# Optimization experiments

Measured on AMD Instinct MI355X. Metric: run time of the kernel, lower is better.

The kernel has to match this reference:

```python
import jax, jax.numpy as jnp
import numpy as np

EMBED_DIM = 128
BATCH = 8
SEQ = 2048


def setup_inputs() -> dict:
    key = jax.random.key(0)
    k1, k2, k3 = jax.random.split(key, 3)
    inputs = jax.random.normal(k1, (BATCH, SEQ, EMBED_DIM), dtype=jnp.float32)
    rotation_params = jax.random.normal(k2, (EMBED_DIM * 3,), dtype=jnp.float32)
    entangle_params = jax.random.normal(k3, (EMBED_DIM,), dtype=jnp.float32)
    return {"inputs": inputs, "rotation_params": rotation_params, "entangle_params": entangle_params}


def reference(inputs, rotation_params, entangle_params):
    d = inputs.shape[-1]
    rot = rotation_params.reshape(d, 3)          # [d, 3]
    ent = entangle_params.reshape(d, 1)          # [d, 1]
    query = inputs @ rot                         # [B, S, 3]
    key = inputs @ ent                           # [B, S, 1]
    # scores: [B, S, S], softmax over last axis
    logits = jnp.einsum('bsk,btk->bst', query, key) / jnp.sqrt(jnp.float32(d))
    scores = jax.nn.softmax(logits, axis=-1)
    return jnp.einsum('bst,btd->bsd', scores, inputs)  # [B, S, d]
```

## Files before the change

### kernel.cpp

```cpp
#include <hip/hip_runtime.h>
#include <cstddef>
#include <cstdint>

#define SS 2048
#define DD 128
#define NB 8

typedef _Float16 half8 __attribute__((ext_vector_type(8)));
typedef __fp16 fp16x2 __attribute__((ext_vector_type(2)));
typedef __attribute__((ext_vector_type(16))) float f32x16;

#if __has_builtin(__builtin_amdgcn_exp2f)
#define EXP2F(x) __builtin_amdgcn_exp2f(x)
#else
#define EXP2F(x) exp2f(x)
#endif

#define WS_A2   0
#define WS_KV   (NB*SS*4)
#define WS_XF   (2*NB*SS*4)
#define BATCH_B (SS*DD*2)
#define WS_NEED (size_t)(WS_XF + (size_t)NB*BATCH_B)
#define WS_KMX  (WS_XF)
#define WS_KMN  (WS_XF + 128)


__global__ __launch_bounds__(256) void prep(
    const float* __restrict__ X, const float* __restrict__ rotp,
    const float* __restrict__ entp, uint8_t* __restrict__ ws, int do_x) {
  __shared__ __align__(16) uint8_t lbuf[128 * 80];
  const int blk = blockIdx.x;
  const int b = blk & 7;
  const int rc = blk >> 3;
  const int tid = threadIdx.x;
  const int d4 = (tid & 31) * 4;
  float* a2out = (float*)(ws + WS_A2);
  float* kout = (float*)(ws + WS_KV);

  const float4 f0 = *reinterpret_cast<const float4*>(rotp + d4 * 3);
  const float4 f1 = *reinterpret_cast<const float4*>(rotp + d4 * 3 + 4);
  const float4 f2 = *reinterpret_cast<const float4*>(rotp + d4 * 3 + 8);
  const float rs0 = f0.x + f0.y + f0.z;
  const float rs1 = f0.w + f1.x + f1.y;
  const float rs2 = f1.z + f1.w + f2.x;
  const float rs3 = f2.y + f2.z + f2.w;
  const float4 e4 = *reinterpret_cast<const float4*>(entp + d4);

#pragma unroll
  for (int rnd = 0; rnd < 4; ++rnd) {
    const int t31 = rnd * 8 + (tid >> 5);
    const int tg = rc * 32 + t31;
    const float4 xv =
        *reinterpret_cast<const float4*>(X + ((size_t)b * SS + tg) * DD + d4);
    float av = xv.x * rs0 + xv.y * rs1 + xv.z * rs2 + xv.w * rs3;
    float kv = xv.x * e4.x + xv.y * e4.y + xv.z * e4.z + xv.w * e4.w;
#pragma unroll
    for (int off = 16; off > 0; off >>= 1) {
      av += __shfl_xor(av, off, 64);
      kv += __shfl_xor(kv, off, 64);
    }
    if ((tid & 31) == 0) {
      a2out[b * SS + tg] = av * (0.08838834764831845f * 1.4426950408889634f);
      kout[b * SS + tg] = kv;
    }
    if (do_x) {
      const float vv[4] = {xv.x, xv.y, xv.z, xv.w};
#pragma unroll
      for (int i = 0; i < 4; ++i)
        *reinterpret_cast<_Float16*>(lbuf + (d4 + i) * 80 + t31 * 2) =
            (_Float16)vv[i];
    }
  }

  if (do_x) {
    __syncthreads();
    const int T = rc >> 2;
    const int wfb = (rc & 3) * 2;
    uint8_t* outb = ws + WS_XF + (size_t)b * BATCH_B + (T * 8 + wfb) * 4096;
    const int nt = tid >> 6;
    const int lane = tid & 63;
    const int hh = lane >> 5;
    const int d = nt * 32 + (lane & 31);
#pragma unroll
    for (int wfl = 0; wfl < 2; ++wfl) {
      const half8 v = *reinterpret_cast<const half8*>(
          lbuf + d * 80 + (wfl * 16 + hh * 8) * 2);
      *reinterpret_cast<half8*>(outb + wfl * 4096 + nt * 1024 + lane * 16) = v;
    }
  }
}

__global__ __launch_bounds__(1024, 4) void attn_mfma(
    const uint8_t* __restrict__ ws, float* __restrict__ out) {
  __shared__ float comb[64 * 128];
  __shared__ float dl[16 * 32];
  __shared__ float smx[16], smn[16];
  const int tid = threadIdx.x;
  const int w = tid >> 6;
  const int lane = tid & 63;
  const int lm = lane & 31;
  const int h = lane >> 5;
  const int mh = w >> 3;
  const int ks = w & 7;
  const int blk = blockIdx.x;
  const int b = blk & 7;
  const int s0 = (blk >> 3) * 64;

  const float* a2 = (const float*)(ws + WS_A2) + b * SS;
  const float* kb = (const float*)(ws + WS_KV) + b * SS;
  const uint8_t* xf = ws + WS_XF + (size_t)b * BATCH_B;

  const float2 k2 = *reinterpret_cast<const float2*>(kb + tid * 2);
  float mx = fmaxf(k2.x, k2.y);
  float mn = fminf(k2.x, k2.y);
#pragma unroll
  for (int off = 32; off > 0; off >>= 1) {
    mx = fmaxf(mx, __shfl_xor(mx, off, 64));
    mn = fminf(mn, __shfl_xor(mn, off, 64));
  }
  if (lane == 0) { smx[w] = mx; smn[w] = mn; }
  const float ga = a2[s0 + mh * 32 + lm];
  __syncthreads();
  mx = smx[0]; mn = smn[0];
#pragma unroll
  for (int q = 1; q < 16; ++q) { mx = fmaxf(mx, smx[q]); mn = fminf(mn, smn[q]); }
  const float gm = fmaxf(ga * mx, ga * mn);
  float gden = 0.0f;

  f32x16 acc[4];
#pragma unroll
  for (int nt = 0; nt < 4; ++nt)
#pragma unroll
    for (int r = 0; r < 16; ++r) acc[nt][r] = 0.0f;

  const uint8_t* wb = xf + ks * 4096 + lane * 16;
  const float* kp0 = kb + ks * 16 + h * 8;

  half8 bfA[4], bfB[4];
#pragma unroll
  for (int nt = 0; nt < 4; ++nt)
    bfA[nt] = *reinterpret_cast<const half8*>(wb + nt * 1024);

#define ABODY(TT, BFP, BFN)                                                   \
  {                                                                           \
    if ((TT) + 1 < 16) {                                                      \
      const uint8_t* nb_ = wb + ((TT) + 1) * 32768;                           \
      _Pragma("unroll") for (int nt = 0; nt < 4; ++nt)                        \
          BFN[nt] = *reinterpret_cast<const half8*>(nb_ + nt * 1024);         \
    }                                                                         \
    const float* kp = kp0 + (TT) * 128;                                       \
    const float4 ka = *reinterpret_cast<const float4*>(kp);                   \
    const float4 kc = *reinterpret_cast<const float4*>(kp + 4);               \
    const float kv8[8] = {ka.x, ka.y, ka.z, ka.w, kc.x, kc.y, kc.z, kc.w};    \
    float e0[8];                                                              \
    _Pragma("unroll") for (int j = 0; j < 8; ++j) {                           \
      e0[j] = EXP2F(fmaf(ga, kv8[j], -gm));                                   \
      gden += e0[j];                                                          \
    }                                                                         \
    union { half8 v; fp16x2 p[4]; } wa;                                       \
    _Pragma("unroll") for (int q = 0; q < 4; ++q)                             \
        wa.p[q] = __builtin_amdgcn_cvt_pkrtz(e0[2 * q], e0[2 * q + 1]);       \
    __builtin_amdgcn_s_setprio(1);                                            \
    _Pragma("unroll") for (int nt = 0; nt < 4; ++nt)                          \
        acc[nt] = __builtin_amdgcn_mfma_f32_32x32x16_f16(wa.v, BFP[nt],       \
                                                         acc[nt], 0, 0, 0);   \
    __builtin_amdgcn_s_setprio(0);                                            \
  }

  for (int T = 0; T < 16; T += 2) {
    ABODY(T, bfA, bfB);
    ABODY(T + 1, bfB, bfA);
  }
#undef ABODY

  gden += __shfl_xor(gden, 32, 64);
  if (lane < 32) dl[w * 32 + lane] = gden;
#pragma unroll
  for (int p = 0; p < 8; ++p) {
    if (ks == p) {
#pragma unroll
      for (int nt = 0; nt < 4; ++nt)
#pragma unroll
        for (int r = 0; r < 16; ++r) {
          const int rr = (r & 3) + 8 * (r >> 2) + 4 * h;
          const int idx = (mh * 32 + rr) * 128 + nt * 32 + lm;
          if (p == 0) comb[idx] = acc[nt][r];
          else        comb[idx] += acc[nt][r];
        }
    }
    __syncthreads();
  }

  const int r = tid >> 4;
  const int cg = (tid & 15) * 8;
  const int rmh = r >> 5, rm = r & 31;
  float den = 0.0f;
#pragma unroll
  for (int q = 0; q < 8; ++q) den += dl[(rmh * 8 + q) * 32 + rm];
  const float inv = 1.0f / den;
  float* orow = out + ((size_t)b * SS + s0 + r) * DD + cg;
#pragma unroll
  for (int q = 0; q < 2; ++q) {
    float4 v = *reinterpret_cast<const float4*>(&comb[r * 128 + cg + q * 4]);
    v.x *= inv; v.y *= inv; v.z *= inv; v.w *= inv;
    *reinterpret_cast<float4*>(orow + q * 4) = v;
  }
}

__global__ __launch_bounds__(256) void kminmax(const float* __restrict__ kvec,
                                               float* __restrict__ kmx,
                                               float* __restrict__ kmn) {
  const int b = blockIdx.x;
  const int tid = threadIdx.x;
  float mx = -1e30f, mn = 1e30f;
  for (int i = tid; i < SS; i += 256) {
    const float v = kvec[b * SS + i];
    mx = fmaxf(mx, v);
    mn = fminf(mn, v);
  }
#pragma unroll
  for (int off = 32; off > 0; off >>= 1) {
    mx = fmaxf(mx, __shfl_xor(mx, off, 64));
    mn = fminf(mn, __shfl_xor(mn, off, 64));
  }
  __shared__ float smx[4], smn[4];
  const int wid = tid >> 6, lane = tid & 63;
  if (lane == 0) { smx[wid] = mx; smn[wid] = mn; }
  __syncthreads();
  if (tid == 0) {
    kmx[b] = fmaxf(fmaxf(smx[0], smx[1]), fmaxf(smx[2], smx[3]));
    kmn[b] = fminf(fminf(smn[0], smn[1]), fminf(smn[2], smn[3]));
  }
}

__global__ __launch_bounds__(256) void attn_main(
    const float* __restrict__ X, const float* __restrict__ a2,
    const float* __restrict__ kvec, const float* __restrict__ kmx,
    const float* __restrict__ kmn, float* __restrict__ out) {
  __shared__ float xs[64 * DD];
  __shared__ float wt[64 * 32];
  __shared__ float denp[8 * 32];
  const int tid = threadIdx.x;
  const int tx = tid & 15;
  const int ty = (tid >> 4) & 3;
  const int tz = tid >> 6;
  const int b = blockIdx.y;
  const int s0 = blockIdx.x * 32;
  const int sg = tid & 31;
  const int tq = tid >> 5;
  const float ga = a2[b * SS + s0 + sg];
  const float gm = fmaxf(ga * kmx[b], ga * kmn[b]);
  float gden = 0.0f;
  float acc[8][8];
#pragma unroll
  for (int r = 0; r < 8; ++r)
#pragma unroll
    for (int c = 0; c < 8; ++c) acc[r][c] = 0.0f;
  const float* xb = X + (size_t)b * SS * DD;
  const float* kb = kvec + b * SS;
  for (int t0 = 0; t0 < SS; t0 += 64) {
    __syncthreads();
#pragma unroll
    for (int rnd = 0; rnd < 8; ++rnd) {
      const int idx = rnd * 1024 + tid * 4;
      *reinterpret_cast<float4*>(xs + idx) =
          *reinterpret_cast<const float4*>(xb + t0 * DD + idx);
    }
#pragma unroll
    for (int j = 0; j < 8; ++j) {
      const float kt = kb[t0 + tq * 8 + j];
      const float wv = exp2f(fmaf(ga, kt, -gm));
      wt[(tq * 8 + j) * 32 + sg] = wv;
      gden += wv;
    }
    __syncthreads();
#pragma unroll 4
    for (int ti = 0; ti < 16; ++ti) {
      const int tl = tz * 16 + ti;
      const float4 x0 = *reinterpret_cast<const float4*>(xs + tl * DD + tx * 8);
      const float4 x1 = *reinterpret_cast<const float4*>(xs + tl * DD + tx * 8 + 4);
      const float4 w0 = *reinterpret_cast<const float4*>(wt + tl * 32 + ty * 8);
      const float4 w1 = *reinterpret_cast<const float4*>(wt + tl * 32 + ty * 8 + 4);
      const float xr[8] = {x0.x, x0.y, x0.z, x0.w, x1.x, x1.y, x1.z, x1.w};
      const float wr[8] = {w0.x, w0.y, w0.z, w0.w, w1.x, w1.y, w1.z, w1.w};
#pragma unroll
      for (int r = 0; r < 8; ++r)
#pragma unroll
        for (int c = 0; c < 8; ++c) acc[r][c] = fmaf(wr[r], xr[c], acc[r][c]);
    }
  }
  __syncthreads();
  denp[tq * 32 + sg] = gden;
  for (int p = 1; p < 4; ++p) {
    __syncthreads();
    if (tz == p) {
#pragma unroll
      for (int r = 0; r < 8; ++r) {
        const int sl = ty * 8 + r;
        *reinterpret_cast<float4*>(xs + sl * DD + tx * 8) =
            make_float4(acc[r][0], acc[r][1], acc[r][2], acc[r][3]);
        *reinterpret_cast<float4*>(xs + sl * DD + tx * 8 + 4) =
            make_float4(acc[r][4], acc[r][5], acc[r][6], acc[r][7]);
      }
    }
    __syncthreads();
    if (tz == 0) {
#pragma unroll
      for (int r = 0; r < 8; ++r) {
        const int sl = ty * 8 + r;
        const float4 v0 = *reinterpret_cast<const float4*>(xs + sl * DD + tx * 8);
        const float4 v1 = *reinterpret_cast<const float4*>(xs + sl * DD + tx * 8 + 4);
        acc[r][0] += v0.x; acc[r][1] += v0.y; acc[r][2] += v0.z; acc[r][3] += v0.w;
        acc[r][4] += v1.x; acc[r][5] += v1.y; acc[r][6] += v1.z; acc[r][7] += v1.w;
      }
    }
  }
  if (tz == 0) {
#pragma unroll
    for (int r = 0; r < 8; ++r) {
      const int sl = ty * 8 + r;
      float den = 0.0f;
#pragma unroll
      for (int q = 0; q < 8; ++q) den += denp[q * 32 + sl];
      const float inv = 1.0f / den;
      float* orow = out + ((size_t)b * SS + s0 + sl) * DD + tx * 8;
      *reinterpret_cast<float4*>(orow) =
          make_float4(acc[r][0] * inv, acc[r][1] * inv, acc[r][2] * inv, acc[r][3] * inv);
      *reinterpret_cast<float4*>(orow + 4) =
          make_float4(acc[r][4] * inv, acc[r][5] * inv, acc[r][6] * inv, acc[r][7] * inv);
    }
  }
}

extern "C" void kernel_launch(void* const* d_in, const int* in_sizes, int n_in,
                              void* d_out, int out_size, void* d_ws, size_t ws_size,
                              hipStream_t stream) {
  const float* X = (const float*)d_in[0];
  const float* rotp = (const float*)d_in[1];
  const float* entp = (const float*)d_in[2];
  float* out = (float*)d_out;
  uint8_t* ws = (uint8_t*)d_ws;

  if (ws_size >= WS_NEED) {
    prep<<<512, 256, 0, stream>>>(X, rotp, entp, ws, 1);
    attn_mfma<<<256, 1024, 0, stream>>>((const uint8_t*)ws, out);
  } else {
    float* a2 = (float*)(ws + WS_A2);
    float* kv = (float*)(ws + WS_KV);
    float* kmxp = (float*)(ws + WS_KMX);
    float* kmnp = (float*)(ws + WS_KMN);
    prep<<<512, 256, 0, stream>>>(X, rotp, entp, ws, 0);
    kminmax<<<NB, 256, 0, stream>>>(kv, kmxp, kmnp);
    attn_main<<<dim3(SS / 32, NB), 256, 0, stream>>>(X, a2, kv, kmxp, kmnp, out);
  }
}
```

Baseline: 32.61 us.

## Stage B fragments through double-buffered LDS via global_load_lds

Each x tile is now loaded once per workgroup from global memory straight into a double-buffered 64 KB LDS region using global_load_lds. Waves then read their B fragments from LDS, where before each wave did its own register prefetch from global memory. This removes the duplicate global loads made by the two wave groups that share the same ks slice. The cost is a __syncthreads on every one of the 16 tile iterations, extra LDS reads, and a larger shared allocation that is also reused for the combine buffer.

```diff
diff --git a/kernel.cpp b/kernel.cpp
--- a/kernel.cpp
+++ b/kernel.cpp
@@ -90,9 +90,15 @@
   }
 }
 
+typedef __attribute__((address_space(3))) unsigned int lds_u32;
+typedef const __attribute__((address_space(1))) unsigned int glb_u32;
+__device__ __forceinline__ void gload16(const void* g, void* l) {
+  __builtin_amdgcn_global_load_lds((glb_u32*)g, (lds_u32*)l, 16, 0, 0);
+}
+
 __global__ __launch_bounds__(1024, 4) void attn_mfma(
     const uint8_t* __restrict__ ws, float* __restrict__ out) {
-  __shared__ float comb[64 * 128];
+  __shared__ __align__(16) uint8_t smem[65536];
   __shared__ float dl[16 * 32];
   __shared__ float smx[16], smn[16];
   const int tid = threadIdx.x;
@@ -110,6 +116,9 @@
   const float* kb = (const float*)(ws + WS_KV) + b * SS;
   const uint8_t* xf = ws + WS_XF + (size_t)b * BATCH_B;
 
+  gload16(xf + w * 2048 + lane * 16, smem + w * 2048);
+  gload16(xf + w * 2048 + 1024 + lane * 16, smem + w * 2048 + 1024);
+
   const float2 k2 = *reinterpret_cast<const float2*>(kb + tid * 2);
   float mx = fmaxf(k2.x, k2.y);
   float mn = fminf(k2.x, k2.y);
@@ -133,46 +142,43 @@
 #pragma unroll
     for (int r = 0; r < 16; ++r) acc[nt][r] = 0.0f;
 
-  const uint8_t* wb = xf + ks * 4096 + lane * 16;
   const float* kp0 = kb + ks * 16 + h * 8;
-
-  half8 bfA[4], bfB[4];
-#pragma unroll
-  for (int nt = 0; nt < 4; ++nt)
-    bfA[nt] = *reinterpret_cast<const half8*>(wb + nt * 1024);
-
-#define ABODY(TT, BFP, BFN)                                                   \
-  {                                                                           \
-    if ((TT) + 1 < 16) {                                                      \
-      const uint8_t* nb_ = wb + ((TT) + 1) * 32768;                           \
-      _Pragma("unroll") for (int nt = 0; nt < 4; ++nt)                        \
-          BFN[nt] = *reinterpret_cast<const half8*>(nb_ + nt * 1024);         \
-    }                                                                         \
-    const float* kp = kp0 + (TT) * 128;                                       \
-    const float4 ka = *reinterpret_cast<const float4*>(kp);                   \
-    const float4 kc = *reinterpret_cast<const float4*>(kp + 4);               \
-    const float kv8[8] = {ka.x, ka.y, ka.z, ka.w, kc.x, kc.y, kc.z, kc.w};    \
-    float e0[8];                                                              \
-    _Pragma("unroll") for (int j = 0; j < 8; ++j) {                           \
-      e0[j] = EXP2F(fmaf(ga, kv8[j], -gm));                                   \
-      gden += e0[j];                                                          \
-    }                                                                         \
-    union { half8 v; fp16x2 p[4]; } wa;                                       \
-    _Pragma("unroll") for (int q = 0; q < 4; ++q)                             \
-        wa.p[q] = __builtin_amdgcn_cvt_pkrtz(e0[2 * q], e0[2 * q + 1]);       \
-    __builtin_amdgcn_s_setprio(1);                                            \
-    _Pragma("unroll") for (int nt = 0; nt < 4; ++nt)                          \
-        acc[nt] = __builtin_amdgcn_mfma_f32_32x32x16_f16(wa.v, BFP[nt],       \
-                                                         acc[nt], 0, 0, 0);   \
-    __builtin_amdgcn_s_setprio(0);                                            \
-  }
-
-  for (int T = 0; T < 16; T += 2) {
-    ABODY(T, bfA, bfB);
-    ABODY(T + 1, bfB, bfA);
-  }
-#undef ABODY
-
+  int cur = 0;
+
+  for (int T = 0; T < 16; ++T) {
+    if (T < 15) {
+      const uint8_t* nb_ = xf + (size_t)(T + 1) * 32768;
+      const int bb = (cur ^ 1) << 15;
+      gload16(nb_ + w * 2048 + lane * 16, smem + bb + w * 2048);
+      gload16(nb_ + w * 2048 + 1024 + lane * 16, smem + bb + w * 2048 + 1024);
+    }
+    const float* kp = kp0 + T * 128;
+    const float4 ka = *reinterpret_cast<const float4*>(kp);
+    const float4 kc = *reinterpret_cast<const float4*>(kp + 4);
+    const float kv8[8] = {ka.x, ka.y, ka.z, ka.w, kc.x, kc.y, kc.z, kc.w};
+    float e0[8];
+#pragma unroll
+    for (int j = 0; j < 8; ++j) {
+      e0[j] = EXP2F(fmaf(ga, kv8[j], -gm));
+      gden += e0[j];
+    }
+    union { half8 v; fp16x2 p[4]; } wa;
+#pragma unroll
+    for (int q = 0; q < 4; ++q)
+      wa.p[q] = __builtin_amdgcn_cvt_pkrtz(e0[2 * q], e0[2 * q + 1]);
+    const uint8_t* bbuf = smem + (cur << 15) + ks * 4096 + lane * 16;
+    __builtin_amdgcn_s_setprio(1);
+#pragma unroll
+    for (int nt = 0; nt < 4; ++nt) {
+      const half8 bf = *reinterpret_cast<const half8*>(bbuf + nt * 1024);
+      acc[nt] = __builtin_amdgcn_mfma_f32_32x32x16_f16(wa.v, bf, acc[nt], 0, 0, 0);
+    }
+    __builtin_amdgcn_s_setprio(0);
+    __syncthreads();
+    cur ^= 1;
+  }
+
+  float* comb = reinterpret_cast<float*>(smem);
   gden += __shfl_xor(gden, 32, 64);
   if (lane < 32) dl[w * 32 + lane] = gden;
 #pragma unroll
```

New measurement: 31.11 us. 1.05x faster.
